# Kernel optimization log

Measured on AMD Instinct MI355X. Metric: run time of the kernel, lower is better.

The kernel has to match this reference:

```python
import jax, jax.numpy as jnp
import numpy as np

DEPTH = 4  # 2**DEPTH - 1 = 15 decision nodes, 2**DEPTH = 16 leaves


def setup_inputs() -> dict:
    key = jax.random.key(0)
    k1, k2, k3, k4, k5 = jax.random.split(key, 5)
    B, S, H = 2, 2048, 1024
    n_dec, n_leaf = 2 ** DEPTH - 1, 2 ** DEPTH
    s = 1.0 / np.sqrt(H)
    return {
        "x": jax.random.normal(k1, (B, S, H), dtype=jnp.float32),
        "Wd": jax.random.normal(k2, (n_dec, H, 2), dtype=jnp.float32) * s,
        "bd": jax.random.normal(k3, (n_dec, 2), dtype=jnp.float32) * s,
        "Wl": jax.random.normal(k4, (n_leaf, H, H), dtype=jnp.float32) * s,
        "bl": jax.random.normal(k5, (n_leaf, H), dtype=jnp.float32) * s,
    }


def reference(x, Wd, bd, Wl, bl):
    B, S, H = x.shape
    # All decision nodes in one grouped GEMM: [B,S,n_dec,2], independent sigmoids
    decisions = jax.nn.sigmoid(jnp.einsum('bsh,nhk->bsnk', x, Wd) + bd)
    # Cumulative path probabilities with torch-faithful cat([p*left, p*right]) ordering
    path = jnp.ones((B, S, 1), dtype=x.dtype)
    for level in range(DEPTH):
        start = 2 ** level - 1
        lv = decisions[:, :, start:start + 2 ** level, :]  # [B,S,2^level,2]
        path = jnp.concatenate([path * lv[..., 0], path * lv[..., 1]], axis=-1)
    # Weighted leaf-output sum without materializing [B,S,n_leaf,H]
    out = jnp.einsum('bsh,lhd,bsl->bsd', x, Wl, path, optimize=True)
    out = out + jnp.einsum('bsl,ld->bsd', path, bl)
    return out
```

## Files before the change

### kernel.cpp

```cpp
#include <hip/hip_runtime.h>
#include <hip/hip_bf16.h>

typedef unsigned short u16;
typedef unsigned int u32;
typedef short bf16x8 __attribute__((ext_vector_type(8)));
typedef _Float16 f16x8 __attribute__((ext_vector_type(8)));
typedef float f32x4 __attribute__((ext_vector_type(4)));

__device__ __forceinline__ u16 f2bf(float f) {
    u32 u = __builtin_bit_cast(u32, f);
    u32 r = (u + 0x7FFFu + ((u >> 16) & 1u)) >> 16;
    return (u16)r;
}
__device__ __forceinline__ u16 f2h(float f) {
    _Float16 h = (_Float16)f;
    return __builtin_bit_cast(u16, h);
}

__device__ __forceinline__ void lds16(const void* g, void* s) {
    __builtin_amdgcn_global_load_lds(
        (const __attribute__((address_space(1))) u32*)g,
        (__attribute__((address_space(3))) u32*)s, 16, 0, 0);
}

__global__ __launch_bounds__(256) void path_kernel(
    const float* __restrict__ x, const float* __restrict__ Wd,
    const float* __restrict__ bd, float* __restrict__ path,
    u16* __restrict__ xb, int as_f16, int M) {
    int lane = threadIdx.x & 63;
    int wid = threadIdx.x >> 6;
    int m = blockIdx.x * 4 + wid;
    if (m >= M) return;

    const float* xr = x + (size_t)m * 1024;
    float v[16];
#pragma unroll
    for (int i = 0; i < 16; ++i) v[i] = xr[lane + 64 * i];
#pragma unroll
    for (int i = 0; i < 16; ++i)
        xb[(size_t)m * 1024 + lane + 64 * i] = as_f16 ? f2h(v[i]) : f2bf(v[i]);

    int leaf = lane & 15;
    int nd[4], bit[4];
#pragma unroll
    for (int k = 0; k < 4; ++k) {
        nd[k] = (1 << k) - 1 + (leaf & ((1 << k) - 1));
        bit[k] = (leaf >> k) & 1;
    }
    float z[4] = {0.f, 0.f, 0.f, 0.f};

    const float2* Wd2 = (const float2*)Wd;
    for (int n = 0; n < 15; ++n) {
        float s0 = 0.f, s1 = 0.f;
#pragma unroll
        for (int i = 0; i < 16; ++i) {
            float2 w = Wd2[n * 1024 + lane + 64 * i];
            s0 += v[i] * w.x;
            s1 += v[i] * w.y;
        }
#pragma unroll
        for (int off = 32; off; off >>= 1) {
            s0 += __shfl_xor(s0, off, 64);
            s1 += __shfl_xor(s1, off, 64);
        }
#pragma unroll
        for (int k = 0; k < 4; ++k)
            if (nd[k] == n) z[k] = bit[k] ? s1 : s0;
    }
    float p = 1.f;
#pragma unroll
    for (int k = 0; k < 4; ++k) {
        float zz = z[k] + bd[nd[k] * 2 + bit[k]];
        p *= 1.f / (1.f + expf(-zz));
    }
    if (lane < 16) path[(size_t)m * 16 + leaf] = p;
}

__global__ __launch_bounds__(256) void wlt_kernel(
    const float* __restrict__ Wl, u16* __restrict__ wlt, int as_f16) {
    __shared__ float tile[64][65];
    int l = blockIdx.z, hb = blockIdx.y, nb = blockIdx.x;
    int t = threadIdx.x;
    int r = t >> 2, cq = (t & 3) << 4;

    const float* src = Wl + ((size_t)(l * 1024 + hb * 64 + r)) * 1024 + nb * 64 + cq;
#pragma unroll
    for (int j = 0; j < 4; ++j) {
        float4 w = ((const float4*)src)[j];
        tile[r][cq + 4 * j + 0] = w.x;
        tile[r][cq + 4 * j + 1] = w.y;
        tile[r][cq + 4 * j + 2] = w.z;
        tile[r][cq + 4 * j + 3] = w.w;
    }
    __syncthreads();
    union { u16 u[16]; uint4 q[2]; } pk;
#pragma unroll
    for (int j = 0; j < 16; ++j)
        pk.u[j] = as_f16 ? f2h(tile[cq + j][r]) : f2bf(tile[cq + j][r]);
    u16* dst = wlt + ((size_t)(l * 1024 + nb * 64 + r)) * 1024 + hb * 64 + cq;
    ((uint4*)dst)[0] = pk.q[0];
    ((uint4*)dst)[1] = pk.q[1];
}

__global__ __launch_bounds__(512, 2) void tree_gemm8(
    const u16* __restrict__ xh, const u16* __restrict__ wlt,
    const float* __restrict__ path, float* __restrict__ out,
    float* __restrict__ part, int M) {
    __shared__ __align__(16) u16 Asm[2][2][128 * 64];
    __shared__ __align__(16) u16 Bsm[2][2][128 * 64];
    __shared__ u16 psm_h[4][256];

    const int tid = threadIdx.x, lane = tid & 63, w = tid >> 6;
    const int wm = w >> 2, wn = w & 3;
    const int nbm = M >> 8;
    int xb_, yb_, zb_;
    {
        int bid = blockIdx.x;
        if ((nbm << 4) == 256) {
            int k = bid & 7, s = bid >> 3;
            zb_ = k >> 1; yb_ = (k & 1) * 8 + (s >> 2); xb_ = s & 3;
        } else {
            xb_ = bid & 3; int t2 = bid >> 2; yb_ = t2 % nbm; zb_ = t2 / nbm;
        }
    }
    const int n0 = xb_ * 256, m0 = yb_ * 256, z = zb_;
    const int z4 = z * 4;
    const int rl = lane >> 3;
    const int srcswz = ((lane & 7) ^ rl) << 4;
    const int arow = (lane & 15) * 128;
    const int coff0 = ((lane >> 4) << 4) ^ ((lane & 7) << 4);

    for (int i = tid; i < 1024; i += 512) {
        int r = i >> 2, lz = i & 3;
        psm_h[lz][r] = f2h(path[(size_t)(m0 + r) * 16 + z4 + lz]);
    }

#define ISSUE_A(dst_, ks_)                                                          \
    {                                                                               \
        _Pragma("unroll") for (int h_ = 0; h_ < 2; ++h_)                            \
        _Pragma("unroll") for (int j_ = 0; j_ < 2; ++j_)                            \
            lds16((const char*)xh +                                                 \
                      (size_t)(m0 + h_ * 128 + w * 16 + j_ * 8 + rl) * 2048 +       \
                      ((ks_) << 7) + srcswz,                                        \
                  (dst_) + h_ * 16384 + w * 2048 + j_ * 1024);                      \
    }
#define ISSUE_B(dst_, t_)                                                           \
    if ((t_) < 64) {                                                                \
        size_t lb_ = (size_t)(z4 + ((t_) & 3)) * 2097152 +                          \
                     ((size_t)((t_) >> 2) << 7);                                    \
        _Pragma("unroll") for (int h_ = 0; h_ < 2; ++h_)                            \
        _Pragma("unroll") for (int j_ = 0; j_ < 2; ++j_)                            \
            lds16((const char*)wlt + lb_ +                                          \
                      (size_t)(n0 + h_ * 128 + w * 16 + j_ * 8 + rl) * 2048 +       \
                      srcswz,                                                       \
                  (dst_) + h_ * 16384 + w * 2048 + j_ * 1024);                      \
    }
#define LDA4(aB_, mfb)                                                              \
    _Pragma("unroll") for (int q_ = 0; q_ < 4; ++q_) {                              \
        aR[q_][0] = *(const f16x8*)((aB_) + ((mfb) + q_) * 2048 + coff0);           \
        aR[q_][1] = *(const f16x8*)((aB_) + ((mfb) + q_) * 2048 + (coff0 ^ 64));    \
    }
#define LDB2(bB_, nfb, d0)                                                          \
    _Pragma("unroll") for (int q_ = 0; q_ < 2; ++q_) {                              \
        bR[(d0) + q_][0] = *(const f16x8*)((bB_) + ((nfb) + q_) * 2048 + coff0);    \
        bR[(d0) + q_][1] =                                                          \
            *(const f16x8*)((bB_) + ((nfb) + q_) * 2048 + (coff0 ^ 64));            \
    }
#define LDP(ll, mfb)                                                                \
    _Pragma("unroll") for (int q_ = 0; q_ < 4; ++q_)                                \
        p2[q_] = __builtin_bit_cast(                                                \
            _Float16, psm_h[ll][wm * 128 + ((mfb) + q_) * 16 + (lane & 15)]);
#define SCALE                                                                       \
    _Pragma("unroll") for (int q_ = 0; q_ < 4; ++q_) {                              \
        aR[q_][0] *= p2[q_];                                                        \
        aR[q_][1] *= p2[q_];                                                        \
    }
#define MM(a0, b0)                                                                  \
    _Pragma("unroll") for (int mq_ = 0; mq_ < 4; ++mq_)                             \
    _Pragma("unroll") for (int nq_ = 0; nq_ < 2; ++nq_) {                           \
        acc[(a0) + mq_][(b0) + nq_] = __builtin_amdgcn_mfma_f32_16x16x32_f16(       \
            aR[mq_][0], bR[(b0) + nq_][0], acc[(a0) + mq_][(b0) + nq_], 0, 0, 0);   \
        acc[(a0) + mq_][(b0) + nq_] = __builtin_amdgcn_mfma_f32_16x16x32_f16(       \
            aR[mq_][1], bR[(b0) + nq_][1], acc[(a0) + mq_][(b0) + nq_], 0, 0, 0);   \
    }
#define BAR __builtin_amdgcn_s_barrier()
#define LG0 asm volatile("s_waitcnt lgkmcnt(0)" ::: "memory")
#define SCHED0 __builtin_amdgcn_sched_barrier(0)
#define PRIO1 __builtin_amdgcn_s_setprio(1)
#define PRIO0 __builtin_amdgcn_s_setprio(0)
#define VM0 asm volatile("s_waitcnt vmcnt(0)" ::: "memory")
#define VM4 asm volatile("s_waitcnt vmcnt(4)" ::: "memory")
#define NOPX ((void)0)

#define TILE(aB_, bB_, ll, EB, EA, WT)                                              \
    {                                                                               \
        f16x8 aR[4][2], bR[4][2];                                                   \
        _Float16 p2[4];                                                             \
        LDA4(aB_, 0); LDB2(bB_, 0, 0); LDB2(bB_, 2, 2); LDP(ll, 0);                 \
        EB; EA;                                                                     \
        LG0; SCHED0;                                                                \
        SCALE;                                                                      \
        PRIO1; MM(0, 0); MM(0, 2); PRIO0;                                           \
        LDA4(aB_, 4); LDP(ll, 4);                                                   \
        LG0; SCHED0;                                                                \
        SCALE;                                                                      \
        PRIO1; MM(4, 0); MM(4, 2); PRIO0;                                           \
        WT; BAR;                                                                    \
    }

    f32x4 acc[8][4];
#pragma unroll
    for (int a = 0; a < 8; ++a)
#pragma unroll
        for (int b = 0; b < 4; ++b) acc[a][b] = (f32x4){0.f, 0.f, 0.f, 0.f};

    const char* aBase0 = (const char*)Asm[0][wm] + arow;
    const char* aBase1 = (const char*)Asm[1][wm] + arow;
    const char* bBase0 = (const char*)Bsm[0][wn >> 1] + (wn & 1) * 8192 + arow;
    const char* bBase1 = (const char*)Bsm[1][wn >> 1] + (wn & 1) * 8192 + arow;
    char* aSlot0 = (char*)Asm[0][0];
    char* aSlot1 = (char*)Asm[1][0];
    char* bSlot0 = (char*)Bsm[0][0];
    char* bSlot1 = (char*)Bsm[1][0];

    ISSUE_A(aSlot0, 0);
    ISSUE_B(bSlot0, 0);
    asm volatile("s_waitcnt vmcnt(0) lgkmcnt(0)" ::: "memory");
    BAR;
    SCHED0;

#pragma unroll 1
    for (int ks = 0; ks < 15; ++ks) {
        const int t4 = ks << 2;
        const char* aB = (ks & 1) ? aBase1 : aBase0;
        char* aD = (ks & 1) ? aSlot0 : aSlot1;
        TILE(aB, bBase0, 0, ISSUE_B(bSlot1, t4 + 1), NOPX, VM0);
        TILE(aB, bBase1, 1, ISSUE_B(bSlot0, t4 + 2), ISSUE_A(aD, ks + 1), VM4);
        TILE(aB, bBase0, 2, ISSUE_B(bSlot1, t4 + 3), NOPX, VM0);
        TILE(aB, bBase1, 3, ISSUE_B(bSlot0, t4 + 4), NOPX, VM0);
    }
    {
        const char* aB = aBase1;
        TILE(aB, bBase0, 0, ISSUE_B(bSlot1, 61), NOPX, VM0);
        TILE(aB, bBase1, 1, ISSUE_B(bSlot0, 62), NOPX, VM0);
        TILE(aB, bBase0, 2, ISSUE_B(bSlot1, 63), NOPX, VM0);
        TILE(aB, bBase1, 3, NOPX, NOPX, NOPX);
    }

    float* po = (z == 0) ? out : part + (size_t)(z - 1) * M * 1024;
    const int r0 = m0 + wm * 128 + ((lane >> 4) << 2);
    const int c0 = n0 + wn * 64 + (lane & 15);
#pragma unroll
    for (int mf = 0; mf < 8; ++mf)
#pragma unroll
        for (int jj = 0; jj < 4; ++jj)
#pragma unroll
            for (int nf = 0; nf < 4; ++nf)
                po[(size_t)(r0 + mf * 16 + jj) * 1024 + c0 + nf * 16] = acc[mf][nf][jj];
#undef ISSUE_A
#undef ISSUE_B
#undef LDA4
#undef LDB2
#undef LDP
#undef SCALE
#undef MM
#undef BAR
#undef LG0
#undef SCHED0
#undef PRIO1
#undef PRIO0
#undef VM0
#undef VM4
#undef NOPX
#undef TILE
}

__global__ __launch_bounds__(256) void tree_gemm_fb(
    const u16* __restrict__ xb, const u16* __restrict__ wlt,
    const float* __restrict__ path, float* __restrict__ pout,
    int M, int LPB, int lgLPB) {
    __shared__ __align__(16) u16 Asm[128 * 64];
    __shared__ __align__(16) u16 Bsm[128 * 64];
    __shared__ float psm[128][16];

    const int tid = threadIdx.x, lane = tid & 63, wid = tid >> 6;
    const int wm = wid >> 1, wn = wid & 1;
    const int m0 = blockIdx.y * 128, n0 = blockIdx.x * 128;
    const int lbase = blockIdx.z * LPB;

    for (int i = tid; i < (128 << lgLPB); i += 256) {
        int r = i >> lgLPB, c = i & (LPB - 1);
        psm[r][c] = path[(size_t)(m0 + r) * 16 + lbase + c];
    }

    const int colb = (((lane & 7) ^ (lane >> 3)) << 4);
    const int rl = lane >> 3;

    f32x4 accF[4][4], accL[4][4];
#pragma unroll
    for (int a = 0; a < 4; ++a)
#pragma unroll
        for (int b = 0; b < 4; ++b) {
            accF[a][b] = (f32x4){0.f, 0.f, 0.f, 0.f};
            accL[a][b] = (f32x4){0.f, 0.f, 0.f, 0.f};
        }

    const int nsteps = LPB << 4;
    for (int sl = 0; sl < nsteps; ++sl) {
        const int l_ = lbase + (sl >> 4);
        const int h2_ = (sl & 15) << 7;
#pragma unroll
        for (int i_ = 0; i_ < 4; ++i_) {
            int seg_ = wid * 4 + i_;
            int r_ = seg_ * 8 + rl;
            lds16((const char*)xb + (size_t)(m0 + r_) * 2048 + h2_ + colb,
                  (char*)Asm + seg_ * 1024);
            lds16((const char*)wlt + (size_t)(l_ * 1024 + n0 + r_) * 2048 + h2_ + colb,
                  (char*)Bsm + seg_ * 1024);
        }
        __syncthreads();

#pragma unroll
        for (int kf = 0; kf < 2; ++kf) {
            int c2 = kf * 64 + ((lane >> 4) << 4);
            bf16x8 af[4], bfr[4];
#pragma unroll
            for (int mf = 0; mf < 4; ++mf) {
                int rr = wm * 64 + mf * 16 + (lane & 15);
                af[mf] = *(const bf16x8*)((const char*)Asm + rr * 128 + (c2 ^ ((lane & 7) << 4)));
            }
#pragma unroll
            for (int nf = 0; nf < 4; ++nf) {
                int rr = wn * 64 + nf * 16 + (lane & 15);
                bfr[nf] = *(const bf16x8*)((const char*)Bsm + rr * 128 + (c2 ^ ((lane & 7) << 4)));
            }
#pragma unroll
            for (int mf = 0; mf < 4; ++mf)
#pragma unroll
                for (int nf = 0; nf < 4; ++nf)
                    accL[mf][nf] = __builtin_amdgcn_mfma_f32_16x16x32_bf16(
                        af[mf], bfr[nf], accL[mf][nf], 0, 0, 0);
        }
        __syncthreads();

        if ((sl & 15) == 15) {
            int ll = sl >> 4;
#pragma unroll
            for (int mf = 0; mf < 4; ++mf)
#pragma unroll
                for (int jj = 0; jj < 4; ++jj) {
                    float p = psm[wm * 64 + mf * 16 + ((lane >> 4) << 2) + jj][ll];
#pragma unroll
                    for (int nf = 0; nf < 4; ++nf) {
                        accF[mf][nf][jj] += p * accL[mf][nf][jj];
                        accL[mf][nf][jj] = 0.f;
                    }
                }
        }
    }

    float* po = pout + (size_t)blockIdx.z * M * 1024;
#pragma unroll
    for (int mf = 0; mf < 4; ++mf)
#pragma unroll
        for (int jj = 0; jj < 4; ++jj) {
            int rowl = wm * 64 + mf * 16 + ((lane >> 4) << 2) + jj;
#pragma unroll
            for (int nf = 0; nf < 4; ++nf) {
                int col = n0 + wn * 64 + nf * 16 + (lane & 15);
                po[(size_t)(m0 + rowl) * 1024 + col] = accF[mf][nf][jj];
            }
        }
}

__global__ __launch_bounds__(256) void reduce_kernel(
    const float* __restrict__ extra, const float* __restrict__ path,
    const float* __restrict__ bl, float* __restrict__ out, int M,
    int nExtra, int readOut) {
    int m = blockIdx.x, t = threadIdx.x;
    size_t i4 = (size_t)m * 256 + t;
    f32x4 acc = {0.f, 0.f, 0.f, 0.f};
    if (readOut) acc = ((const f32x4*)out)[i4];
    for (int g = 0; g < nExtra; ++g)
        acc += ((const f32x4*)extra)[(size_t)g * M * 256 + i4];
#pragma unroll
    for (int l = 0; l < 16; ++l) {
        float p = path[(size_t)m * 16 + l];
        f32x4 b = ((const f32x4*)bl)[l * 256 + t];
        acc += p * b;
    }
    ((f32x4*)out)[i4] = acc;
}

extern "C" void kernel_launch(void* const* d_in, const int* in_sizes, int n_in,
                              void* d_out, int out_size, void* d_ws, size_t ws_size,
                              hipStream_t stream) {
    const float* x  = (const float*)d_in[0];
    const float* Wd = (const float*)d_in[1];
    const float* bd = (const float*)d_in[2];
    const float* Wl = (const float*)d_in[3];
    const float* bl = (const float*)d_in[4];
    float* out = (float*)d_out;

    const int H = 1024;
    const int M = in_sizes[0] / H;
    char* ws = (char*)d_ws;

    size_t n_off_xh   = (size_t)M * 16 * 4;
    size_t n_off_wlt  = n_off_xh + (size_t)M * 1024 * 2;
    size_t n_off_part = n_off_wlt + (size_t)16 * 1024 * 1024 * 2;
    size_t n_need     = n_off_part + 3 * (size_t)M * 1024 * 4;

    if (ws_size >= n_need && (M % 256) == 0) {
        float* path = (float*)ws;
        u16* xh  = (u16*)(ws + n_off_xh);
        u16* wlt = (u16*)(ws + n_off_wlt);
        float* part = (float*)(ws + n_off_part);

        path_kernel<<<M / 4, 256, 0, stream>>>(x, Wd, bd, path, xh, 1, M);
        wlt_kernel<<<dim3(16, 16, 16), 256, 0, stream>>>(Wl, wlt, 1);
        tree_gemm8<<<4 * (M / 256) * 4, 512, 0, stream>>>(xh, wlt, path, out, part, M);
        reduce_kernel<<<M, 256, 0, stream>>>(part, path, bl, out, M, 3, 1);
        return;
    }

    size_t off_xb   = (size_t)M * 16 * 4;
    size_t off_wlt  = off_xb + (size_t)M * 1024 * 2;
    size_t off_part = off_wlt + (size_t)16 * 1024 * 1024 * 2;
    size_t per_part = (size_t)M * 1024 * 4;

    int G = 1;
    if (ws_size >= off_part + 4 * per_part) G = 4;
    else if (ws_size >= off_part + 2 * per_part) G = 2;
    const int LPB = 16 / G;
    const int lgLPB = (G == 1) ? 4 : (G == 2) ? 3 : 2;

    float* path = (float*)ws;
    u16* xb  = (u16*)(ws + off_xb);
    u16* wlt = (u16*)(ws + off_wlt);
    float* pout = (G == 1) ? out : (float*)(ws + off_part);

    path_kernel<<<M / 4, 256, 0, stream>>>(x, Wd, bd, path, xb, 0, M);
    wlt_kernel<<<dim3(16, 16, 16), 256, 0, stream>>>(Wl, wlt, 0);
    tree_gemm_fb<<<dim3(8, M / 128, G), 256, 0, stream>>>(xb, wlt, path, pout, M, LPB, lgLPB);
    reduce_kernel<<<M, 256, 0, stream>>>(pout, path, bl, out, M,
                                         (G == 1) ? 0 : G, (G == 1) ? 1 : 0);
}
```

Baseline: 197.3 us.

## Remap warps to 4x2 grid and keep A fragments resident across leaf tiles

Changes the per-warp output tile from 128x64 to 64x128 (4 rows by 2 columns of warps). Each warp now loads its A fragments once per K step into registers and reuses them across the four leaf sub-tiles, so only B fragments stream from LDS. The B loads are double-buffered with partial lgkmcnt waits so they overlap the MFMAs. All path probabilities are preloaded into registers once, and the A operand is scaled per leaf on the fly. The cost is more live registers (resident A, preloaded path values, two B buffers), which could cause spills under the 512-thread launch bound.

```diff
diff --git a/kernel.cpp b/kernel.cpp
--- a/kernel.cpp
+++ b/kernel.cpp
@@ -111,7 +111,7 @@
     __shared__ u16 psm_h[4][256];
 
     const int tid = threadIdx.x, lane = tid & 63, w = tid >> 6;
-    const int wm = w >> 2, wn = w & 3;
+    const int wm = w >> 1, wn = w & 1;
     const int nbm = M >> 8;
     int xb_, yb_, zb_;
     {
@@ -155,36 +155,31 @@
                       srcswz,                                                       \
                   (dst_) + h_ * 16384 + w * 2048 + j_ * 1024);                      \
     }
-#define LDA4(aB_, mfb)                                                              \
+#define LDAU(aB_)                                                                   \
     _Pragma("unroll") for (int q_ = 0; q_ < 4; ++q_) {                              \
-        aR[q_][0] = *(const f16x8*)((aB_) + ((mfb) + q_) * 2048 + coff0);           \
-        aR[q_][1] = *(const f16x8*)((aB_) + ((mfb) + q_) * 2048 + (coff0 ^ 64));    \
-    }
-#define LDB2(bB_, nfb, d0)                                                          \
+        aU[q_][0] = *(const f16x8*)((aB_) + q_ * 2048 + coff0);                     \
+        aU[q_][1] = *(const f16x8*)((aB_) + q_ * 2048 + (coff0 ^ 64));              \
+    }
+#define LDBJ(dst_, bB_, j_)                                                         \
     _Pragma("unroll") for (int q_ = 0; q_ < 2; ++q_) {                              \
-        bR[(d0) + q_][0] = *(const f16x8*)((bB_) + ((nfb) + q_) * 2048 + coff0);    \
-        bR[(d0) + q_][1] =                                                          \
-            *(const f16x8*)((bB_) + ((nfb) + q_) * 2048 + (coff0 ^ 64));            \
-    }
-#define LDP(ll, mfb)                                                                \
-    _Pragma("unroll") for (int q_ = 0; q_ < 4; ++q_)                                \
-        p2[q_] = __builtin_bit_cast(                                                \
-            _Float16, psm_h[ll][wm * 128 + ((mfb) + q_) * 16 + (lane & 15)]);
-#define SCALE                                                                       \
-    _Pragma("unroll") for (int q_ = 0; q_ < 4; ++q_) {                              \
-        aR[q_][0] *= p2[q_];                                                        \
-        aR[q_][1] *= p2[q_];                                                        \
-    }
-#define MM(a0, b0)                                                                  \
-    _Pragma("unroll") for (int mq_ = 0; mq_ < 4; ++mq_)                             \
-    _Pragma("unroll") for (int nq_ = 0; nq_ < 2; ++nq_) {                           \
-        acc[(a0) + mq_][(b0) + nq_] = __builtin_amdgcn_mfma_f32_16x16x32_f16(       \
-            aR[mq_][0], bR[(b0) + nq_][0], acc[(a0) + mq_][(b0) + nq_], 0, 0, 0);   \
-        acc[(a0) + mq_][(b0) + nq_] = __builtin_amdgcn_mfma_f32_16x16x32_f16(       \
-            aR[mq_][1], bR[(b0) + nq_][1], acc[(a0) + mq_][(b0) + nq_], 0, 0, 0);   \
+        dst_[q_][0] = *(const f16x8*)((bB_) + ((j_)*2 + q_) * 2048 + coff0);        \
+        dst_[q_][1] = *(const f16x8*)((bB_) + ((j_)*2 + q_) * 2048 + (coff0 ^ 64)); \
+    }
+#define QMM(bRx, nb_, ll)                                                           \
+    _Pragma("unroll") for (int mq_ = 0; mq_ < 4; ++mq_) {                           \
+        _Float16 pp_ = pcAll[mq_][ll];                                              \
+        f16x8 s0_ = aU[mq_][0] * pp_;                                               \
+        f16x8 s1_ = aU[mq_][1] * pp_;                                               \
+        _Pragma("unroll") for (int nq_ = 0; nq_ < 2; ++nq_) {                       \
+            acc[mq_][(nb_) + nq_] = __builtin_amdgcn_mfma_f32_16x16x32_f16(         \
+                s0_, bRx[nq_][0], acc[mq_][(nb_) + nq_], 0, 0, 0);                  \
+            acc[mq_][(nb_) + nq_] = __builtin_amdgcn_mfma_f32_16x16x32_f16(         \
+                s1_, bRx[nq_][1], acc[mq_][(nb_) + nq_], 0, 0, 0);                  \
+        }                                                                           \
     }
 #define BAR __builtin_amdgcn_s_barrier()
-#define LG0 asm volatile("s_waitcnt lgkmcnt(0)" ::: "memory")
+#define LGK0 asm volatile("s_waitcnt lgkmcnt(0)" ::: "memory")
+#define LGK4 asm volatile("s_waitcnt lgkmcnt(4)" ::: "memory")
 #define SCHED0 __builtin_amdgcn_sched_barrier(0)
 #define PRIO1 __builtin_amdgcn_s_setprio(1)
 #define PRIO0 __builtin_amdgcn_s_setprio(0)
@@ -192,32 +187,37 @@
 #define VM4 asm volatile("s_waitcnt vmcnt(4)" ::: "memory")
 #define NOPX ((void)0)
 
-#define TILE(aB_, bB_, ll, EB, EA, WT)                                              \
+#define TILE(aB_, bB_, ll, LA, EB, EA, WT)                                          \
     {                                                                               \
-        f16x8 aR[4][2], bR[4][2];                                                   \
-        _Float16 p2[4];                                                             \
-        LDA4(aB_, 0); LDB2(bB_, 0, 0); LDB2(bB_, 2, 2); LDP(ll, 0);                 \
+        f16x8 bRa[2][2], bRb[2][2];                                                 \
+        LA;                                                  \
+        LDBJ(bRa, bB_, 0);                                                          \
         EB; EA;                                                                     \
-        LG0; SCHED0;                                                                \
-        SCALE;                                                                      \
-        PRIO1; MM(0, 0); MM(0, 2); PRIO0;                                           \
-        LDA4(aB_, 4); LDP(ll, 4);                                                   \
-        LG0; SCHED0;                                                                \
-        SCALE;                                                                      \
-        PRIO1; MM(4, 0); MM(4, 2); PRIO0;                                           \
+        LDBJ(bRb, bB_, 1);                                                          \
+        LGK4; SCHED0;                             \
+        PRIO1; QMM(bRa, 0, ll); PRIO0;                                              \
+        LDBJ(bRa, bB_, 2);                                                          \
+        LGK4; SCHED0;                                  \
+        PRIO1; QMM(bRb, 2, ll); PRIO0;                                              \
+        LDBJ(bRb, bB_, 3);                                                          \
+        LGK4; SCHED0;                                  \
+        PRIO1; QMM(bRa, 4, ll); PRIO0;                                              \
+        LGK0; SCHED0;                                                \
+        PRIO1; QMM(bRb, 6, ll); PRIO0;                                              \
         WT; BAR;                                                                    \
     }
 
-    f32x4 acc[8][4];
-#pragma unroll
-    for (int a = 0; a < 8; ++a)
-#pragma unroll
-        for (int b = 0; b < 4; ++b) acc[a][b] = (f32x4){0.f, 0.f, 0.f, 0.f};
-
-    const char* aBase0 = (const char*)Asm[0][wm] + arow;
-    const char* aBase1 = (const char*)Asm[1][wm] + arow;
-    const char* bBase0 = (const char*)Bsm[0][wn >> 1] + (wn & 1) * 8192 + arow;
-    const char* bBase1 = (const char*)Bsm[1][wn >> 1] + (wn & 1) * 8192 + arow;
+    f32x4 acc[4][8];
+#pragma unroll
+    for (int a = 0; a < 4; ++a)
+#pragma unroll
+        for (int b = 0; b < 8; ++b) acc[a][b] = (f32x4){0.f, 0.f, 0.f, 0.f};
+    f16x8 aU[4][2];
+
+    const char* aBase0 = (const char*)Asm[0][wm >> 1] + (wm & 1) * 8192 + arow;
+    const char* aBase1 = (const char*)Asm[1][wm >> 1] + (wm & 1) * 8192 + arow;
+    const char* bBase0 = (const char*)Bsm[0][wn] + arow;
+    const char* bBase1 = (const char*)Bsm[1][wn] + arow;
     char* aSlot0 = (char*)Asm[0][0];
     char* aSlot1 = (char*)Asm[1][0];
     char* bSlot0 = (char*)Bsm[0][0];
@@ -227,6 +227,14 @@
     ISSUE_B(bSlot0, 0);
     asm volatile("s_waitcnt vmcnt(0) lgkmcnt(0)" ::: "memory");
     BAR;
+
+    _Float16 pcAll[4][4];
+#pragma unroll
+    for (int m_ = 0; m_ < 4; ++m_)
+#pragma unroll
+        for (int l_ = 0; l_ < 4; ++l_)
+            pcAll[m_][l_] = __builtin_bit_cast(
+                _Float16, psm_h[l_][wm * 64 + m_ * 16 + (lane & 15)]);
     SCHED0;
 
 #pragma unroll 1
@@ -234,38 +242,37 @@
         const int t4 = ks << 2;
         const char* aB = (ks & 1) ? aBase1 : aBase0;
         char* aD = (ks & 1) ? aSlot0 : aSlot1;
-        TILE(aB, bBase0, 0, ISSUE_B(bSlot1, t4 + 1), NOPX, VM0);
-        TILE(aB, bBase1, 1, ISSUE_B(bSlot0, t4 + 2), ISSUE_A(aD, ks + 1), VM4);
-        TILE(aB, bBase0, 2, ISSUE_B(bSlot1, t4 + 3), NOPX, VM0);
-        TILE(aB, bBase1, 3, ISSUE_B(bSlot0, t4 + 4), NOPX, VM0);
+        TILE(aB, bBase0, 0, LDAU(aB), ISSUE_B(bSlot1, t4 + 1), NOPX, VM0);
+        TILE(aB, bBase1, 1, NOPX, ISSUE_B(bSlot0, t4 + 2), ISSUE_A(aD, ks + 1), VM4);
+        TILE(aB, bBase0, 2, NOPX, ISSUE_B(bSlot1, t4 + 3), NOPX, VM0);
+        TILE(aB, bBase1, 3, NOPX, ISSUE_B(bSlot0, t4 + 4), NOPX, VM0);
     }
     {
         const char* aB = aBase1;
-        TILE(aB, bBase0, 0, ISSUE_B(bSlot1, 61), NOPX, VM0);
-        TILE(aB, bBase1, 1, ISSUE_B(bSlot0, 62), NOPX, VM0);
-        TILE(aB, bBase0, 2, ISSUE_B(bSlot1, 63), NOPX, VM0);
-        TILE(aB, bBase1, 3, NOPX, NOPX, NOPX);
+        TILE(aB, bBase0, 0, LDAU(aB), ISSUE_B(bSlot1, 61), NOPX, VM0);
+        TILE(aB, bBase1, 1, NOPX, ISSUE_B(bSlot0, 62), NOPX, VM0);
+        TILE(aB, bBase0, 2, NOPX, ISSUE_B(bSlot1, 63), NOPX, VM0);
+        TILE(aB, bBase1, 3, NOPX, NOPX, NOPX, NOPX);
     }
 
     float* po = (z == 0) ? out : part + (size_t)(z - 1) * M * 1024;
-    const int r0 = m0 + wm * 128 + ((lane >> 4) << 2);
-    const int c0 = n0 + wn * 64 + (lane & 15);
-#pragma unroll
-    for (int mf = 0; mf < 8; ++mf)
+    const int r0 = m0 + wm * 64 + ((lane >> 4) << 2);
+    const int c0 = n0 + wn * 128 + (lane & 15);
+#pragma unroll
+    for (int mf = 0; mf < 4; ++mf)
 #pragma unroll
         for (int jj = 0; jj < 4; ++jj)
 #pragma unroll
-            for (int nf = 0; nf < 4; ++nf)
+            for (int nf = 0; nf < 8; ++nf)
                 po[(size_t)(r0 + mf * 16 + jj) * 1024 + c0 + nf * 16] = acc[mf][nf][jj];
 #undef ISSUE_A
 #undef ISSUE_B
-#undef LDA4
-#undef LDB2
-#undef LDP
-#undef SCALE
-#undef MM
+#undef LDAU
+#undef LDBJ
+#undef QMM
 #undef BAR
-#undef LG0
+#undef LGK0
+#undef LGK4
 #undef SCHED0
 #undef PRIO1
 #undef PRIO0
```

Result: slower. 431.4 us (+118.6%).
